# Kernel optimization log

Measured on AMD Instinct MI355X. Metric: run time of the kernel, lower is better.

The kernel has to match this reference:

```python
import jax, jax.numpy as jnp
import numpy as np

T, OBS, H, NOBJ = 32768, 256, 512, 4


def _xavier(key, shape):
    fan_in, fan_out = shape[0], shape[1]
    lim = jnp.sqrt(6.0 / (fan_in + fan_out)).astype(jnp.float32)
    return jax.random.uniform(key, shape, jnp.float32, -lim, lim)


def setup_inputs() -> dict:
    key = jax.random.key(0)
    ks = jax.random.split(key, 16)
    # weights stored as [in, out] so y = x @ W (same math as nn.Linear with W.T)
    return {
        "x": jax.random.normal(ks[0], (T, OBS), jnp.float32),
        "W_in0": _xavier(ks[1], (OBS, H)),
        "W_B0": _xavier(ks[2], (OBS, H)),
        "W_C0": _xavier(ks[3], (OBS, H)),
        "W_d0": _xavier(ks[4], (OBS, H)),
        "A_log0": jax.random.normal(ks[5], (H,), jnp.float32),
        "W_in1": _xavier(ks[6], (H, H)),
        "W_B1": _xavier(ks[7], (H, H)),
        "W_C1": _xavier(ks[8], (H, H)),
        "W_d1": _xavier(ks[9], (H, H)),
        "A_log1": jax.random.normal(ks[10], (H,), jnp.float32),
        "W_out": _xavier(ks[11], (H, NOBJ)),
        "b_out": jnp.zeros((NOBJ,), jnp.float32),
        "W_skip": _xavier(ks[12], (OBS, NOBJ)),
    }


def _mamba_layer(x, W_in, W_B, W_C, W_d, A_log):
    # x: [T, D_in] -> [T, H]
    x_state = x @ W_in           # [T, H]
    B = x @ W_B                  # [T, H]
    C = x @ W_C                  # [T, H]
    delta = jax.nn.sigmoid(x @ W_d)  # [T, H]
    A = -jnp.exp(A_log)          # [H]
    A_bar = jnp.exp(delta * A)   # [T, H], in (0, 1)
    Bx = B * x_state             # [T, H]

    def step(h, inp):
        a_t, bx_t = inp
        h = a_t * h + bx_t
        return h, h

    h0 = jnp.zeros((x_state.shape[-1],), x_state.dtype)
    _, h_seq = jax.lax.scan(step, h0, (A_bar, Bx))  # [T, H]
    return C * h_seq


def reference(x, W_in0, W_B0, W_C0, W_d0, A_log0,
              W_in1, W_B1, W_C1, W_d1, A_log1,
              W_out, b_out, W_skip):
    skip = x
    y = _mamba_layer(x, W_in0, W_B0, W_C0, W_d0, A_log0)
    y = _mamba_layer(y, W_in1, W_B1, W_C1, W_d1, A_log1)
    out = y @ W_out + b_out + skip @ W_skip  # [T, NOBJ]
    return out
```

## Files before the change

### kernel.cpp

```cpp
#include <hip/hip_runtime.h>

typedef __attribute__((ext_vector_type(8))) short short8;
typedef __attribute__((ext_vector_type(4))) float floatx4;

#define T_SIZE 32768
#define OBS    256
#define H      512
#define NC     512
#define CHUNK  64
#define NGRP   64
#define GCH    8
#define SLAB   ((size_t)T_SIZE * 32)

__device__ __forceinline__ unsigned short f2bf(float f){
    union { float f; unsigned u; } v; v.f = f;
    unsigned u = v.u;
    u += 0x7FFFu + ((u >> 16) & 1u);
    return (unsigned short)(u >> 16);
}
__device__ __forceinline__ float bf2f(unsigned short u){
    union { unsigned u; float f; } v; v.u = ((unsigned)u) << 16; return v.f;
}

#define GLOAD_LDS16(g, l) \
    __builtin_amdgcn_global_load_lds((const __attribute__((address_space(1))) unsigned*)(g), \
                                     (__attribute__((address_space(3))) unsigned*)(l), 16, 0, 0)

__global__ void cast_x_kernel(const float* __restrict__ x, unsigned short* __restrict__ xb, int n4){
    int i = blockIdx.x * 256 + threadIdx.x;
    if (i < n4){
        float4 v = ((const float4*)x)[i];
        ushort4 o;
        o.x = f2bf(v.x); o.y = f2bf(v.y); o.z = f2bf(v.z); o.w = f2bf(v.w);
        ((ushort4*)xb)[i] = o;
    }
}

__global__ void tcast4_kernel(const float* __restrict__ W0, const float* __restrict__ W1,
                              const float* __restrict__ W2, const float* __restrict__ W3,
                              unsigned short* __restrict__ dst, int K, int KH){
    int idx = blockIdx.x * 256 + threadIdx.x;
    if (idx >= 4 * KH) return;
    int s   = idx / KH;
    int rem = idx - s * KH;
    int k = rem >> 9;
    int h = rem & 511;
    const float* W = (s == 0) ? W0 : (s == 1) ? W1 : (s == 2) ? W2 : W3;
    int b = h >> 4, hh = h & 15;
    dst[(size_t)((b * 4 + s) * 16 + hh) * K + k] = f2bf(W[(size_t)k * H + h]);
}

__global__ __launch_bounds__(256) void gemm_layer_kernel(
    const unsigned short* __restrict__ xb,
    const unsigned short* __restrict__ wt,
    const float* __restrict__ A_log,
    unsigned short* __restrict__ gT, unsigned short* __restrict__ bxT, unsigned short* __restrict__ CT,
    float* __restrict__ Pbuf, float* __restrict__ Hbuf,
    int K)
{
    __shared__ unsigned short SM[2][8192];

    const int tid  = threadIdx.x;
    const int wave = tid >> 6;
    const int lane = tid & 63;
    const int ml   = lane & 15;
    const int quad = lane >> 4;
    const int wm   = wave & 1;
    const int wn   = wave >> 1;

    const int flat = blockIdx.y * 16 + blockIdx.x;
    const int xcd  = flat & 7;
    const int j    = flat >> 3;
    const int nb   = j & 15;
    const int mb   = (j >> 4) * 8 + xcd;
    const int m0   = mb * 128;

    const int srow = tid >> 2;
    const int sel  = (((tid & 3) ^ ((tid >> 3) & 3))) * 8;
    const int swz  = (ml >> 1) & 3;

    const unsigned short* pa0 = xb + (size_t)(m0 + srow) * K + sel;
    const unsigned short* pa1 = pa0 + (size_t)64 * K;
    const unsigned short* pb0 = wt + (size_t)(nb * 128 + srow) * K + sel;
    const unsigned short* pb1 = pb0 + (size_t)64 * K;

    const int ldsA0 = (wave * 64 + 0  ) * 8;
    const int ldsA1 = (wave * 64 + 256) * 8;

    floatx4 acc[4][4];
    #pragma unroll
    for (int i = 0; i < 4; i++)
        #pragma unroll
        for (int jj = 0; jj < 4; jj++)
            acc[i][jj] = (floatx4)(0.0f);

    GLOAD_LDS16(pa0, &SM[0][ldsA0]);
    GLOAD_LDS16(pa1, &SM[0][ldsA1]);
    GLOAD_LDS16(pb0, &SM[0][4096 + ldsA0]);
    GLOAD_LDS16(pb1, &SM[0][4096 + ldsA1]);

    const int nk = K >> 5;
    for (int kk = 0; kk < nk; ++kk){
        __syncthreads();
        const int cur = kk & 1;
        if (kk + 1 < nk){
            const int nxt = cur ^ 1;
            const int ko  = (kk + 1) * 32;
            GLOAD_LDS16(pa0 + ko, &SM[nxt][ldsA0]);
            GLOAD_LDS16(pa1 + ko, &SM[nxt][ldsA1]);
            GLOAD_LDS16(pb0 + ko, &SM[nxt][4096 + ldsA0]);
            GLOAD_LDS16(pb1 + ko, &SM[nxt][4096 + ldsA1]);
        }

        const unsigned short* As = &SM[cur][0];
        const unsigned short* Bs = &SM[cur][4096];
        short8 av[4], bv[4];
        #pragma unroll
        for (int i = 0; i < 4; i++)
            av[i] = *(const short8*)(As + (size_t)(wm * 64 + i * 16 + ml) * 32 + (quad ^ swz) * 8);
        #pragma unroll
        for (int jj = 0; jj < 4; jj++)
            bv[jj] = *(const short8*)(Bs + (size_t)(wn * 64 + jj * 16 + ml) * 32 + (quad ^ swz) * 8);

        #pragma unroll
        for (int i = 0; i < 4; i++)
            #pragma unroll
            for (int jj = 0; jj < 4; jj++)
                acc[i][jj] = __builtin_amdgcn_mfma_f32_16x16x32_bf16(av[i], bv[jj], acc[i][jj], 0, 0, 0);
    }
    __syncthreads();

    unsigned short* SMe = &SM[0][0];
    const int col = wn * 16 + ml;
    const int h   = nb * 32 + col;
    const float Aneg = -expf(A_log[h]);

    float segp[4], segh[4];
    #pragma unroll
    for (int i = 0; i < 4; i++){
        float p = 1.0f, hh = 0.0f;
        #pragma unroll
        for (int r = 0; r < 4; r++){
            int trow = wm * 64 + i * 16 + quad * 4 + r;
            float dv = acc[i][3][r];
            float delta = 1.0f / (1.0f + expf(-dv));
            unsigned short gb = f2bf(delta * Aneg);
            float a = expf(bf2f(gb));
            unsigned short bb = f2bf(acc[i][1][r] * acc[i][0][r]);
            SMe[        trow * 32 + col] = gb;
            SMe[4096 +  trow * 32 + col] = bb;
            SMe[8192 +  trow * 32 + col] = f2bf(acc[i][2][r]);
            hh = fmaf(a, hh, bf2f(bb));
            p *= a;
        }
        segp[i] = p; segh[i] = hh;
    }
    __syncthreads();
    {
        const short8* s8 = (const short8*)SMe;
        short8* dg = (short8*)(gT  + (size_t)nb * SLAB + (size_t)m0 * 32);
        short8* db = (short8*)(bxT + (size_t)nb * SLAB + (size_t)m0 * 32);
        short8* dc = (short8*)(CT  + (size_t)nb * SLAB + (size_t)m0 * 32);
        dg[tid] = s8[tid];        dg[tid + 256] = s8[tid + 256];
        db[tid] = s8[512 + tid];  db[tid + 256] = s8[768 + tid];
        dc[tid] = s8[1024 + tid]; dc[tid + 256] = s8[1280 + tid];
    }
    __syncthreads();

    float2* segbuf = (float2*)SMe;
    #pragma unroll
    for (int i = 0; i < 4; i++)
        segbuf[(i * 4 + quad) * 64 + col * 2 + wm] = make_float2(segp[i], segh[i]);
    __syncthreads();
    if (tid < 64){
        int ccol = tid >> 1, ch = tid & 1;
        float P = 1.0f, Hc = 0.0f;
        #pragma unroll
        for (int s = 0; s < 16; s++){
            float2 ph = segbuf[s * 64 + ccol * 2 + ch];
            Hc = fmaf(ph.x, Hc, ph.y);
            P *= ph.x;
        }
        int c = mb * 2 + ch;
        Pbuf[(size_t)c * H + nb * 32 + ccol] = P;
        Hbuf[(size_t)c * H + nb * 32 + ccol] = Hc;
    }
}

__global__ void scan2a_kernel(const float* __restrict__ P, const float* __restrict__ Hc,
                              float* __restrict__ Pg, float* __restrict__ Hg){
    const int g  = blockIdx.x;
    const int j4 = threadIdx.x * 4;
    float4 pc = {1.f,1.f,1.f,1.f}, hc = {0.f,0.f,0.f,0.f};
    #pragma unroll
    for (int i = 0; i < GCH; i++){
        size_t o = (size_t)(g * GCH + i) * H + j4;
        float4 P4 = *(const float4*)(P + o);
        float4 H4 = *(const float4*)(Hc + o);
        hc.x = fmaf(P4.x, hc.x, H4.x); pc.x *= P4.x;
        hc.y = fmaf(P4.y, hc.y, H4.y); pc.y *= P4.y;
        hc.z = fmaf(P4.z, hc.z, H4.z); pc.z *= P4.z;
        hc.w = fmaf(P4.w, hc.w, H4.w); pc.w *= P4.w;
    }
    *(float4*)(Pg + (size_t)g * H + j4) = pc;
    *(float4*)(Hg + (size_t)g * H + j4) = hc;
}

__global__ void scan2b_kernel(const float* __restrict__ Pg, const float* __restrict__ Hg,
                              float* __restrict__ Cg){
    const int j = threadIdx.x;
    float carry = 0.0f;
    for (int g0 = 0; g0 < NGRP; g0 += 8){
        float p[8], h[8];
        #pragma unroll
        for (int i = 0; i < 8; i++){
            p[i] = Pg[(size_t)(g0 + i) * H + j];
            h[i] = Hg[(size_t)(g0 + i) * H + j];
        }
        #pragma unroll
        for (int i = 0; i < 8; i++){
            Cg[(size_t)(g0 + i) * H + j] = carry;
            carry = fmaf(p[i], carry, h[i]);
        }
    }
}

__global__ void scan3_kernel(const unsigned short* __restrict__ gT, const unsigned short* __restrict__ bxT,
                             const unsigned short* __restrict__ CT,
                             const float* __restrict__ P, const float* __restrict__ Hc,
                             const float* __restrict__ Cg,
                             unsigned short* __restrict__ yb){
    int idx = blockIdx.x * 256 + threadIdx.x;
    int j4 = (idx & 127) * 4;
    int c  = idx >> 7;
    int nb = j4 >> 5, jj = j4 & 31;
    int grp = c >> 3;
    float4 h = *(const float4*)(Cg + (size_t)grp * H + j4);
    for (int cc = grp << 3; cc < c; ++cc){
        float4 P4 = *(const float4*)(P + (size_t)cc * H + j4);
        float4 H4 = *(const float4*)(Hc + (size_t)cc * H + j4);
        h.x = fmaf(P4.x, h.x, H4.x);
        h.y = fmaf(P4.y, h.y, H4.y);
        h.z = fmaf(P4.z, h.z, H4.z);
        h.w = fmaf(P4.w, h.w, H4.w);
    }
    size_t off = (size_t)nb * SLAB + (size_t)c * CHUNK * 32 + jj;
    size_t yo  = (size_t)c * CHUNK * H + j4;
    #pragma unroll 8
    for (int i = 0; i < CHUNK; i++){
        ushort4 gv = *(const ushort4*)(gT + off);
        ushort4 bv = *(const ushort4*)(bxT + off);
        ushort4 cv = *(const ushort4*)(CT + off);
        h.x = fmaf(expf(bf2f(gv.x)), h.x, bf2f(bv.x));
        h.y = fmaf(expf(bf2f(gv.y)), h.y, bf2f(bv.y));
        h.z = fmaf(expf(bf2f(gv.z)), h.z, bf2f(bv.z));
        h.w = fmaf(expf(bf2f(gv.w)), h.w, bf2f(bv.w));
        ushort4 o;
        o.x = f2bf(bf2f(cv.x) * h.x);
        o.y = f2bf(bf2f(cv.y) * h.y);
        o.z = f2bf(bf2f(cv.z) * h.z);
        o.w = f2bf(bf2f(cv.w) * h.w);
        *(ushort4*)(yb + yo) = o;
        off += 32; yo += H;
    }
}

__global__ __launch_bounds__(256) void final_kernel(const unsigned short* __restrict__ y2,
                                                    const unsigned short* __restrict__ xb,
                                                    const float* __restrict__ Wout,
                                                    const float* __restrict__ bout,
                                                    const float* __restrict__ Wskip,
                                                    float* __restrict__ out){
    int wave = threadIdx.x >> 6;
    int lane = threadIdx.x & 63;
    int t = blockIdx.x * 4 + wave;
    float s0 = 0.f, s1 = 0.f, s2 = 0.f, s3 = 0.f;
    const float4* W4 = (const float4*)Wout;
    #pragma unroll
    for (int k = lane; k < H; k += 64){
        float yv = bf2f(y2[(size_t)t * H + k]);
        float4 w = W4[k];
        s0 = fmaf(yv, w.x, s0); s1 = fmaf(yv, w.y, s1);
        s2 = fmaf(yv, w.z, s2); s3 = fmaf(yv, w.w, s3);
    }
    const float4* S4 = (const float4*)Wskip;
    #pragma unroll
    for (int k = lane; k < OBS; k += 64){
        float xv = bf2f(xb[(size_t)t * OBS + k]);
        float4 w = S4[k];
        s0 = fmaf(xv, w.x, s0); s1 = fmaf(xv, w.y, s1);
        s2 = fmaf(xv, w.z, s2); s3 = fmaf(xv, w.w, s3);
    }
    #pragma unroll
    for (int off = 32; off > 0; off >>= 1){
        s0 += __shfl_down(s0, off);
        s1 += __shfl_down(s1, off);
        s2 += __shfl_down(s2, off);
        s3 += __shfl_down(s3, off);
    }
    if (lane == 0){
        out[(size_t)t * 4 + 0] = s0 + bout[0];
        out[(size_t)t * 4 + 1] = s1 + bout[1];
        out[(size_t)t * 4 + 2] = s2 + bout[2];
        out[(size_t)t * 4 + 3] = s3 + bout[3];
    }
}

extern "C" void kernel_launch(void* const* d_in, const int* in_sizes, int n_in,
                              void* d_out, int out_size, void* d_ws, size_t ws_size,
                              hipStream_t stream)
{
    const float* x     = (const float*)d_in[0];
    const float* W_in0 = (const float*)d_in[1];
    const float* W_B0  = (const float*)d_in[2];
    const float* W_C0  = (const float*)d_in[3];
    const float* W_d0  = (const float*)d_in[4];
    const float* A0    = (const float*)d_in[5];
    const float* W_in1 = (const float*)d_in[6];
    const float* W_B1  = (const float*)d_in[7];
    const float* W_C1  = (const float*)d_in[8];
    const float* W_d1  = (const float*)d_in[9];
    const float* A1    = (const float*)d_in[10];
    const float* Wout  = (const float*)d_in[11];
    const float* bout  = (const float*)d_in[12];
    const float* Wskip = (const float*)d_in[13];
    float* out = (float*)d_out;

    char* ws = (char*)d_ws;
    size_t off = 0;
    auto alloc = [&](size_t bytes) -> void* {
        void* p = ws + off;
        off += (bytes + 255) & ~(size_t)255;
        return p;
    };
    unsigned short* xb  = (unsigned short*)alloc((size_t)T_SIZE * OBS * 2);
    unsigned short* yb  = (unsigned short*)alloc((size_t)T_SIZE * H * 2);
    unsigned short* Wt0 = (unsigned short*)alloc((size_t)4 * H * OBS * 2);
    unsigned short* Wt1 = (unsigned short*)alloc((size_t)4 * H * H * 2);
    unsigned short* gT  = (unsigned short*)alloc((size_t)T_SIZE * H * 2);
    unsigned short* bxT = (unsigned short*)alloc((size_t)T_SIZE * H * 2);
    unsigned short* CT  = (unsigned short*)alloc((size_t)T_SIZE * H * 2);
    float* Pbuf = (float*)alloc((size_t)NC * H * 4);
    float* Hbuf = (float*)alloc((size_t)NC * H * 4);
    float* Pg   = (float*)alloc((size_t)NGRP * H * 4);
    float* Hg   = (float*)alloc((size_t)NGRP * H * 4);
    float* Cg   = (float*)alloc((size_t)NGRP * H * 4);
    (void)ws_size; (void)in_sizes; (void)n_in; (void)out_size;

    cast_x_kernel<<<(T_SIZE * OBS / 4 + 255) / 256, 256, 0, stream>>>(x, xb, T_SIZE * OBS / 4);
    tcast4_kernel<<<(4 * OBS * H + 255) / 256, 256, 0, stream>>>(W_in0, W_B0, W_C0, W_d0, Wt0, OBS, OBS * H);
    tcast4_kernel<<<(4 * H   * H + 255) / 256, 256, 0, stream>>>(W_in1, W_B1, W_C1, W_d1, Wt1, H,   H * H);

    dim3 ggrid(16, 256);
    const int sgrid = NC * 128 / 256;

    gemm_layer_kernel<<<ggrid, 256, 0, stream>>>(xb, Wt0, A0, gT, bxT, CT, Pbuf, Hbuf, OBS);
    scan2a_kernel<<<NGRP, 128, 0, stream>>>(Pbuf, Hbuf, Pg, Hg);
    scan2b_kernel<<<1, H, 0, stream>>>(Pg, Hg, Cg);
    scan3_kernel<<<sgrid, 256, 0, stream>>>(gT, bxT, CT, Pbuf, Hbuf, Cg, yb);

    gemm_layer_kernel<<<ggrid, 256, 0, stream>>>(yb, Wt1, A1, gT, bxT, CT, Pbuf, Hbuf, H);
    scan2a_kernel<<<NGRP, 128, 0, stream>>>(Pbuf, Hbuf, Pg, Hg);
    scan2b_kernel<<<1, H, 0, stream>>>(Pg, Hg, Cg);
    scan3_kernel<<<sgrid, 256, 0, stream>>>(gT, bxT, CT, Pbuf, Hbuf, Cg, yb );

    final_kernel<<<T_SIZE / 4, 256, 0, stream>>>(yb, xb, Wout, bout, Wskip, out);
}
```

Measured before the change: 347.6 us.

## Triple-buffer GEMM LDS loads with prefetch depth two and explicit waitcnts

The GEMM main loop moves from double to triple buffering in LDS, keeping two k-tiles of global-to-LDS loads in flight. The __syncthreads plus implicit full wait is replaced by an lgkmcnt wait, a raw s_barrier and vmcnt(8), so only the oldest tile's loads must finish. The epilogue also writes segment products straight into a separate LDS buffer, removing two barriers. This costs 16KB more LDS per block, which may lower occupancy, and it issues redundant clamped loads of the last tile.

New measurement: 357.4 us. 1.03x slower.

```diff
diff --git a/kernel.cpp b/kernel.cpp
--- a/kernel.cpp
+++ b/kernel.cpp
@@ -58,7 +58,7 @@
     float* __restrict__ Pbuf, float* __restrict__ Hbuf,
     int K)
 {
-    __shared__ unsigned short SM[2][8192];
+    __shared__ unsigned short SM[3][8192];
 
     const int tid  = threadIdx.x;
     const int wave = tid >> 6;
@@ -94,26 +94,32 @@
         for (int jj = 0; jj < 4; jj++)
             acc[i][jj] = (floatx4)(0.0f);
 
-    GLOAD_LDS16(pa0, &SM[0][ldsA0]);
-    GLOAD_LDS16(pa1, &SM[0][ldsA1]);
-    GLOAD_LDS16(pb0, &SM[0][4096 + ldsA0]);
-    GLOAD_LDS16(pb1, &SM[0][4096 + ldsA1]);
-
     const int nk = K >> 5;
+    GLOAD_LDS16(pa0,      &SM[0][ldsA0]);
+    GLOAD_LDS16(pa1,      &SM[0][ldsA1]);
+    GLOAD_LDS16(pb0,      &SM[0][4096 + ldsA0]);
+    GLOAD_LDS16(pb1,      &SM[0][4096 + ldsA1]);
+    GLOAD_LDS16(pa0 + 32, &SM[1][ldsA0]);
+    GLOAD_LDS16(pa1 + 32, &SM[1][ldsA1]);
+    GLOAD_LDS16(pb0 + 32, &SM[1][4096 + ldsA0]);
+    GLOAD_LDS16(pb1 + 32, &SM[1][4096 + ldsA1]);
+
+    int rd = 0, wr = 2;
     for (int kk = 0; kk < nk; ++kk){
-        __syncthreads();
-        const int cur = kk & 1;
-        if (kk + 1 < nk){
-            const int nxt = cur ^ 1;
-            const int ko  = (kk + 1) * 32;
-            GLOAD_LDS16(pa0 + ko, &SM[nxt][ldsA0]);
-            GLOAD_LDS16(pa1 + ko, &SM[nxt][ldsA1]);
-            GLOAD_LDS16(pb0 + ko, &SM[nxt][4096 + ldsA0]);
-            GLOAD_LDS16(pb1 + ko, &SM[nxt][4096 + ldsA1]);
-        }
-
-        const unsigned short* As = &SM[cur][0];
-        const unsigned short* Bs = &SM[cur][4096];
+        asm volatile("s_waitcnt lgkmcnt(0)" ::: "memory");
+        asm volatile("s_barrier" ::: "memory");
+
+        const int kf = (kk + 2 < nk) ? (kk + 2) : (nk - 1);
+        const int ko = kf * 32;
+        GLOAD_LDS16(pa0 + ko, &SM[wr][ldsA0]);
+        GLOAD_LDS16(pa1 + ko, &SM[wr][ldsA1]);
+        GLOAD_LDS16(pb0 + ko, &SM[wr][4096 + ldsA0]);
+        GLOAD_LDS16(pb1 + ko, &SM[wr][4096 + ldsA1]);
+
+        asm volatile("s_waitcnt vmcnt(8)" ::: "memory");
+
+        const unsigned short* As = &SM[rd][0];
+        const unsigned short* Bs = &SM[rd][4096];
         short8 av[4], bv[4];
         #pragma unroll
         for (int i = 0; i < 4; i++)
@@ -127,15 +133,21 @@
             #pragma unroll
             for (int jj = 0; jj < 4; jj++)
                 acc[i][jj] = __builtin_amdgcn_mfma_f32_16x16x32_bf16(av[i], bv[jj], acc[i][jj], 0, 0, 0);
-    }
+
+        const int tmp = rd;
+        rd = (rd == 2) ? 0 : rd + 1;
+        wr = tmp;
+    }
+    asm volatile("s_waitcnt lgkmcnt(0)" ::: "memory");
+    asm volatile("s_waitcnt vmcnt(0)" ::: "memory");
     __syncthreads();
 
     unsigned short* SMe = &SM[0][0];
+    float2* segbuf = (float2*)(&SM[2][0]);
     const int col = wn * 16 + ml;
     const int h   = nb * 32 + col;
     const float Aneg = -expf(A_log[h]);
 
-    float segp[4], segh[4];
     #pragma unroll
     for (int i = 0; i < 4; i++){
         float p = 1.0f, hh = 0.0f;
@@ -153,7 +165,7 @@
             hh = fmaf(a, hh, bf2f(bb));
             p *= a;
         }
-        segp[i] = p; segh[i] = hh;
+        segbuf[(i * 4 + quad) * 64 + col * 2 + wm] = make_float2(p, hh);
     }
     __syncthreads();
     {
@@ -165,13 +177,6 @@
         db[tid] = s8[512 + tid];  db[tid + 256] = s8[768 + tid];
         dc[tid] = s8[1024 + tid]; dc[tid + 256] = s8[1280 + tid];
     }
-    __syncthreads();
-
-    float2* segbuf = (float2*)SMe;
-    #pragma unroll
-    for (int i = 0; i < 4; i++)
-        segbuf[(i * 4 + quad) * 64 + col * 2 + wm] = make_float2(segp[i], segh[i]);
-    __syncthreads();
     if (tid < 64){
         int ccol = tid >> 1, ch = tid & 1;
         float P = 1.0f, Hc = 0.0f;
```

## Halve scan chunk size to double scan parallelism and template GEMM on K

Applied to the files above, without the earlier changes.

Shrinks the scan chunk from 64 to 32 timesteps, which doubles the number of chunks and so the number of threads in the sequential scan3 pass. The GEMM epilogue now emits four chunk summaries per 128-row tile and writes them to a separate region of shared memory, which removes a barrier. The GEMM is templated on K so its k-loop can be fully unrolled. The cost is more chunk-carry work in scan2a/scan3 and a larger unrolled GEMM body.

After: 334.2 us. 1.04x faster.

```diff
diff --git a/kernel.cpp b/kernel.cpp
--- a/kernel.cpp
+++ b/kernel.cpp
@@ -6,10 +6,10 @@
 #define T_SIZE 32768
 #define OBS    256
 #define H      512
-#define NC     512
-#define CHUNK  64
+#define NC     1024
+#define CHUNK  32
 #define NGRP   64
-#define GCH    8
+#define GCH    16
 #define SLAB   ((size_t)T_SIZE * 32)
 
 __device__ __forceinline__ unsigned short f2bf(float f){
@@ -50,13 +50,13 @@
     dst[(size_t)((b * 4 + s) * 16 + hh) * K + k] = f2bf(W[(size_t)k * H + h]);
 }
 
+template<int K>
 __global__ __launch_bounds__(256) void gemm_layer_kernel(
     const unsigned short* __restrict__ xb,
     const unsigned short* __restrict__ wt,
     const float* __restrict__ A_log,
     unsigned short* __restrict__ gT, unsigned short* __restrict__ bxT, unsigned short* __restrict__ CT,
-    float* __restrict__ Pbuf, float* __restrict__ Hbuf,
-    int K)
+    float* __restrict__ Pbuf, float* __restrict__ Hbuf)
 {
     __shared__ unsigned short SM[2][8192];
 
@@ -87,6 +87,9 @@
     const int ldsA0 = (wave * 64 + 0  ) * 8;
     const int ldsA1 = (wave * 64 + 256) * 8;
 
+    const int rbaseA = (wm * 64 + ml) * 32 + (quad ^ swz) * 8;
+    const int rbaseB = (wn * 64 + ml) * 32 + (quad ^ swz) * 8;
+
     floatx4 acc[4][4];
     #pragma unroll
     for (int i = 0; i < 4; i++)
@@ -94,16 +97,18 @@
         for (int jj = 0; jj < 4; jj++)
             acc[i][jj] = (floatx4)(0.0f);
 
+    constexpr int NK = K >> 5;
     GLOAD_LDS16(pa0, &SM[0][ldsA0]);
     GLOAD_LDS16(pa1, &SM[0][ldsA1]);
     GLOAD_LDS16(pb0, &SM[0][4096 + ldsA0]);
     GLOAD_LDS16(pb1, &SM[0][4096 + ldsA1]);
 
-    const int nk = K >> 5;
-    for (int kk = 0; kk < nk; ++kk){
+    #pragma unroll
+    for (int kk = 0; kk < NK; ++kk){
         __syncthreads();
+        constexpr_if_helper:;
         const int cur = kk & 1;
-        if (kk + 1 < nk){
+        if (kk + 1 < NK){
             const int nxt = cur ^ 1;
             const int ko  = (kk + 1) * 32;
             GLOAD_LDS16(pa0 + ko, &SM[nxt][ldsA0]);
@@ -112,15 +117,13 @@
             GLOAD_LDS16(pb1 + ko, &SM[nxt][4096 + ldsA1]);
         }
 
-        const unsigned short* As = &SM[cur][0];
-        const unsigned short* Bs = &SM[cur][4096];
         short8 av[4], bv[4];
         #pragma unroll
         for (int i = 0; i < 4; i++)
-            av[i] = *(const short8*)(As + (size_t)(wm * 64 + i * 16 + ml) * 32 + (quad ^ swz) * 8);
+            av[i] = *(const short8*)(&SM[cur][0] + rbaseA + i * 16 * 32);
         #pragma unroll
         for (int jj = 0; jj < 4; jj++)
-            bv[jj] = *(const short8*)(Bs + (size_t)(wn * 64 + jj * 16 + ml) * 32 + (quad ^ swz) * 8);
+            bv[jj] = *(const short8*)(&SM[cur][4096] + rbaseB + jj * 16 * 32);
 
         #pragma unroll
         for (int i = 0; i < 4; i++)
@@ -131,11 +134,11 @@
     __syncthreads();
 
     unsigned short* SMe = &SM[0][0];
+    float2* segbuf = (float2*)(SMe + 12288);
     const int col = wn * 16 + ml;
     const int h   = nb * 32 + col;
     const float Aneg = -expf(A_log[h]);
 
-    float segp[4], segh[4];
     #pragma unroll
     for (int i = 0; i < 4; i++){
         float p = 1.0f, hh = 0.0f;
@@ -153,7 +156,9 @@
             hh = fmaf(a, hh, bf2f(bb));
             p *= a;
         }
-        segp[i] = p; segh[i] = hh;
+        const int ch = wm * 2 + (i >> 1);
+        const int s  = (i & 1) * 4 + quad;
+        segbuf[(ch * 8 + s) * 32 + col] = make_float2(p, hh);
     }
     __syncthreads();
     {
@@ -165,23 +170,16 @@
         db[tid] = s8[512 + tid];  db[tid + 256] = s8[768 + tid];
         dc[tid] = s8[1024 + tid]; dc[tid + 256] = s8[1280 + tid];
     }
-    __syncthreads();
-
-    float2* segbuf = (float2*)SMe;
-    #pragma unroll
-    for (int i = 0; i < 4; i++)
-        segbuf[(i * 4 + quad) * 64 + col * 2 + wm] = make_float2(segp[i], segh[i]);
-    __syncthreads();
-    if (tid < 64){
-        int ccol = tid >> 1, ch = tid & 1;
+    if (tid < 128){
+        const int ccol = tid & 31, ch = tid >> 5;
         float P = 1.0f, Hc = 0.0f;
         #pragma unroll
-        for (int s = 0; s < 16; s++){
-            float2 ph = segbuf[s * 64 + ccol * 2 + ch];
+        for (int s = 0; s < 8; s++){
+            float2 ph = segbuf[(ch * 8 + s) * 32 + ccol];
             Hc = fmaf(ph.x, Hc, ph.y);
             P *= ph.x;
         }
-        int c = mb * 2 + ch;
+        const int c = mb * 4 + ch;
         Pbuf[(size_t)c * H + nb * 32 + ccol] = P;
         Hbuf[(size_t)c * H + nb * 32 + ccol] = Hc;
     }
@@ -234,9 +232,9 @@
     int j4 = (idx & 127) * 4;
     int c  = idx >> 7;
     int nb = j4 >> 5, jj = j4 & 31;
-    int grp = c >> 3;
+    int grp = c >> 4;
     float4 h = *(const float4*)(Cg + (size_t)grp * H + j4);
-    for (int cc = grp << 3; cc < c; ++cc){
+    for (int cc = grp << 4; cc < c; ++cc){
         float4 P4 = *(const float4*)(P + (size_t)cc * H + j4);
         float4 H4 = *(const float4*)(Hc + (size_t)cc * H + j4);
         h.x = fmaf(P4.x, h.x, H4.x);
@@ -354,12 +352,12 @@
     dim3 ggrid(16, 256);
     const int sgrid = NC * 128 / 256;
 
-    gemm_layer_kernel<<<ggrid, 256, 0, stream>>>(xb, Wt0, A0, gT, bxT, CT, Pbuf, Hbuf, OBS);
+    gemm_layer_kernel<OBS><<<ggrid, 256, 0, stream>>>(xb, Wt0, A0, gT, bxT, CT, Pbuf, Hbuf);
     scan2a_kernel<<<NGRP, 128, 0, stream>>>(Pbuf, Hbuf, Pg, Hg);
     scan2b_kernel<<<1, H, 0, stream>>>(Pg, Hg, Cg);
     scan3_kernel<<<sgrid, 256, 0, stream>>>(gT, bxT, CT, Pbuf, Hbuf, Cg, yb);
 
-    gemm_layer_kernel<<<ggrid, 256, 0, stream>>>(yb, Wt1, A1, gT, bxT, CT, Pbuf, Hbuf, H);
+    gemm_layer_kernel<H><<<ggrid, 256, 0, stream>>>(yb, Wt1, A1, gT, bxT, CT, Pbuf, Hbuf);
     scan2a_kernel<<<NGRP, 128, 0, stream>>>(Pbuf, Hbuf, Pg, Hg);
     scan2b_kernel<<<1, H, 0, stream>>>(Pg, Hg, Cg);
     scan3_kernel<<<sgrid, 256, 0, stream>>>(gT, bxT, CT, Pbuf, Hbuf, Cg, yb );
```
